# Performance work log

Measured on AMD Instinct MI355X. Metric: run time of the kernel, lower is better.

The kernel has to match this reference:

```python
import jax, jax.numpy as jnp
import numpy as np

HEADS = 16
PHI = (1.0 + np.sqrt(5.0)) / 2.0


def setup_inputs() -> dict:
    key = jax.random.key(0)
    k1, k2, k3, k4 = jax.random.split(key, 4)
    B, L, D = 2, 2048, 1024
    x = jax.random.normal(k1, (B, L, D), dtype=jnp.float32)
    # nn.Linear(dim, 3*dim, bias=False): store as [D, 3D] for x @ W
    w_qkv = jax.random.normal(k2, (D, 3 * D), dtype=jnp.float32) * (D ** -0.5)
    w_proj = jax.random.normal(k3, (D, D), dtype=jnp.float32) * (D ** -0.5)
    b_proj = jax.random.normal(k4, (D,), dtype=jnp.float32) * 0.01
    return {"x": x, "w_qkv": w_qkv, "w_proj": w_proj, "b_proj": b_proj}


def phi_bias(L):
    # pos[i] = (i * phi) mod 1 ; bias = log(exp(-|pos_i - pos_j|) + 1e-8)
    pos = (jnp.arange(L, dtype=jnp.float32) * PHI) % 1.0
    dist = jnp.abs(pos[:, None] - pos[None, :])  # [L, L]
    return jnp.log(jnp.exp(-dist) + 1e-8)


def reference(x, w_qkv, w_proj, b_proj):
    B, L, D = x.shape
    H = HEADS
    Dh = D // H
    scale = Dh ** -0.5
    qkv = (x @ w_qkv).reshape(B, L, 3, H, Dh)
    q = jnp.transpose(qkv[:, :, 0], (0, 2, 1, 3))  # [B, H, L, Dh]
    k = jnp.transpose(qkv[:, :, 1], (0, 2, 1, 3))
    v = jnp.transpose(qkv[:, :, 2], (0, 2, 1, 3))
    attn = jnp.einsum("bhid,bhjd->bhij", q, k) * scale  # [B, H, L, L]
    attn = attn + phi_bias(L)[None, None]  # additive phi-distance bias
    attn = jax.nn.softmax(attn, axis=-1)
    out = jnp.einsum("bhij,bhjd->bhid", attn, v)  # [B, H, L, Dh]
    out = jnp.transpose(out, (0, 2, 1, 3)).reshape(B, L, D)
    return out @ w_proj + b_proj
```

## Files before the change

kernel.cpp:

```cpp
#include <hip/hip_runtime.h>
#include <math.h>


typedef _Float16 f16;
typedef _Float16 f16x4 __attribute__((ext_vector_type(4)));
typedef _Float16 f16x8 __attribute__((ext_vector_type(8)));
typedef float f32x4 __attribute__((ext_vector_type(4)));

#define MFMA32(a, b, c) __builtin_amdgcn_mfma_f32_16x16x32_f16(a, b, c, 0, 0, 0)

static constexpr int Bsz = 2, Lseq = 2048, Dm = 1024, H = 16, Dh = 64;
static constexpr int Mtot = Bsz * Lseq;
static constexpr int NQKV = 3 * Dm;
static constexpr float PHI_F = 1.61803398874989484820f;
static constexpr float LOG2E = 1.44269504088896f;
static constexpr float QS = 0.125f * LOG2E;
static constexpr float CSTEP = 0.55417527999932633f;

__device__ __forceinline__ void load16_to_lds(const f16* g, f16* l) {
  __builtin_amdgcn_global_load_lds(
      (const __attribute__((address_space(1))) unsigned int*)g,
      (__attribute__((address_space(3))) unsigned int*)l, 16, 0, 0);
}

__global__ __launch_bounds__(256) void cast_f32_f16(const float* __restrict__ in,
                                                    f16* __restrict__ out, int n) {
  int i = (blockIdx.x * 256 + threadIdx.x) * 4;
  if (i < n) {
    float4 v = *reinterpret_cast<const float4*>(in + i);
    f16 t[4] = {(f16)v.x, (f16)v.y, (f16)v.z, (f16)v.w};
    *reinterpret_cast<uint2*>(out + i) = *reinterpret_cast<uint2*>(t);
  }
}

__global__ __launch_bounds__(256) void transpose_cast(const float* __restrict__ in,
                                                      f16* __restrict__ out,
                                                      int K, int N) {
  __shared__ float tile[32][33];
  int n0 = blockIdx.x * 32, k0 = blockIdx.y * 32;
  int tx = threadIdx.x & 31, ty = threadIdx.x >> 5;
#pragma unroll
  for (int r = 0; r < 32; r += 8)
    tile[ty + r][tx] = in[(size_t)(k0 + ty + r) * N + n0 + tx];
  __syncthreads();
#pragma unroll
  for (int r = 0; r < 32; r += 8)
    out[(size_t)(n0 + ty + r) * K + k0 + tx] = (f16)tile[tx][ty + r];
}

__global__ __launch_bounds__(256) void v_transpose(const f16* __restrict__ in,
                                                   f16* __restrict__ out) {
  __shared__ f16 td[64][68];
  int bh = blockIdx.y, l0 = blockIdx.x * 64;
  int tid = threadIdx.x;
  const f16* src = in + (size_t)bh * Lseq * Dh;
#pragma unroll
  for (int c = tid; c < 512; c += 256) {
    int row = c >> 3, col = (c & 7) * 8;
    uint4 v = *reinterpret_cast<const uint4*>(src + (size_t)(l0 + row) * Dh + col);
    f16 tmp[8];
    *reinterpret_cast<uint4*>(tmp) = v;
#pragma unroll
    for (int j = 0; j < 8; j++) td[col + j][row] = tmp[j];
  }
  __syncthreads();
  f16* dst = out + (size_t)bh * Dh * Lseq;
#pragma unroll
  for (int c = tid; c < 512; c += 256) {
    int d = c >> 3, co = c & 7;
    int jh = co >> 2, qd = co & 3;
    f16 tmp[8];
#pragma unroll
    for (int e = 0; e < 4; e++) tmp[e] = td[d][jh * 32 + qd * 4 + e];
#pragma unroll
    for (int e = 0; e < 4; e++) tmp[4 + e] = td[d][jh * 32 + 16 + qd * 4 + e];
    *reinterpret_cast<uint4*>(dst + (size_t)d * Lseq + l0 + co * 8) =
        *reinterpret_cast<uint4*>(tmp);
  }
}

template <int MODE>
__global__ __launch_bounds__(256) void gemm_f16(
    const f16* __restrict__ A, const f16* __restrict__ Bt,
    int M, int N, int K,
    f16* __restrict__ qb, f16* __restrict__ kb, f16* __restrict__ vl,
    float* __restrict__ out, const float* __restrict__ bias) {
  constexpr int BM = (MODE == 0) ? 128 : 64;
  constexpr int MI = BM / 32;
  constexpr int AI = BM / 32;
  __shared__ f16 As[BM * 64];
  __shared__ f16 Bs[128 * 64];

  int tid = threadIdx.x;
  int wave = tid >> 6, lane = tid & 63;
  int quad = lane >> 4, l16 = lane & 15;
  int wm = (wave >> 1) * (MI * 16), wn = (wave & 1) * 64;

  int lid = blockIdx.x;
  int xcd = lid & 7, t = lid >> 3;
  int m0, n0;
  if (MODE == 0) {
    int mg = xcd >> 1, ng = xcd & 1;
    m0 = (mg * 8 + t / 12) * 128;
    n0 = (ng * 12 + t % 12) * 128;
  } else {
    m0 = (xcd * 8 + (t >> 3)) * 64;
    n0 = (t & 7) * 128;
  }

  const int gu = (lane & 7) ^ (lane >> 3);
  const f16* gA[AI];
  f16* lA[AI];
#pragma unroll
  for (int i = 0; i < AI; i++) {
    int it = wave * AI + i;
    gA[i] = A + (size_t)(m0 + it * 8 + (lane >> 3)) * K + gu * 8;
    lA[i] = As + it * 512;
  }
  const f16* gB[4];
  f16* lB[4];
#pragma unroll
  for (int i = 0; i < 4; i++) {
    int it = wave * 4 + i;
    gB[i] = Bt + (size_t)(n0 + it * 8 + (lane >> 3)) * K + gu * 8;
    lB[i] = Bs + it * 512;
  }

  f32x4 acc[MI][4] = {};

  for (int k0 = 0; k0 < K; k0 += 64) {
#pragma unroll
    for (int i = 0; i < AI; i++) load16_to_lds(gA[i] + k0, lA[i]);
#pragma unroll
    for (int i = 0; i < 4; i++) load16_to_lds(gB[i] + k0, lB[i]);
    __syncthreads();
#pragma unroll
    for (int s = 0; s < 2; s++) {
      f16x8 a[MI], b[4];
#pragma unroll
      for (int i = 0; i < MI; i++) {
        int row = wm + i * 16 + l16;
        a[i] = *reinterpret_cast<const f16x8*>(
            As + row * 64 + (((s * 4 + quad) ^ (l16 & 7)) * 8));
      }
#pragma unroll
      for (int j = 0; j < 4; j++) {
        int row = wn + j * 16 + l16;
        b[j] = *reinterpret_cast<const f16x8*>(
            Bs + row * 64 + (((s * 4 + quad) ^ (l16 & 7)) * 8));
      }
#pragma unroll
      for (int i = 0; i < MI; i++)
#pragma unroll
        for (int j = 0; j < 4; j++)
          acc[i][j] = MFMA32(a[i], b[j], acc[i][j]);
    }
    __syncthreads();
  }

#pragma unroll
  for (int i = 0; i < MI; i++) {
#pragma unroll
    for (int j = 0; j < 4; j++) {
      int n = n0 + wn + j * 16 + l16;
#pragma unroll
      for (int r = 0; r < 4; r++) {
        int m = m0 + wm + i * 16 + quad * 4 + r;
        if (MODE == 0) {
          int ty = n >> 10;
          int df = n & 1023;
          int h = df >> 6, dh = df & 63;
          int b = m >> 11, l = m & 2047;
          size_t idx = (((size_t)(b * H + h)) * Lseq + l) * Dh + dh;
          if (ty == 0)
            qb[idx] = (f16)(acc[i][j][r] * QS);
          else if (ty == 1)
            kb[idx] = (f16)acc[i][j][r];
          else
            vl[idx] = (f16)acc[i][j][r];
        } else {
          out[(size_t)m * N + n] = acc[i][j][r] + bias[n];
        }
      }
    }
  }
}

__global__ __launch_bounds__(256, 4) void attn_kernel(
    const f16* __restrict__ qb,
    const f16* __restrict__ kb,
    const f16* __restrict__ vb,
    f16* __restrict__ ctx) {
  __shared__ __align__(16) unsigned char smem[16640];
  f16* Ks = (f16*)smem;
  f16* Vs = (f16*)(smem + 8192);

  int bh = blockIdx.y;
  int q0 = blockIdx.x * 64;
  int tid = threadIdx.x, wave = tid >> 6, lane = tid & 63;
  int quad = lane >> 4, l16 = lane & 15;
  int jhalf = wave >> 1, qhalf = wave & 1;

  f16x8 qfrag[2][2];
  float pq[2];
#pragma unroll
  for (int set = 0; set < 2; set++) {
    int q = q0 + qhalf * 32 + set * 16 + l16;
    const f16* Qrow = qb + ((size_t)bh * Lseq + q) * Dh;
    qfrag[set][0] = *reinterpret_cast<const f16x8*>(Qrow + quad * 8);
    qfrag[set][1] = *reinterpret_cast<const f16x8*>(Qrow + 32 + quad * 8);
    pq[set] = fmodf((float)q * PHI_F, 1.0f);
  }

  float pk[2][4];
#pragma unroll
  for (int jb = 0; jb < 2; jb++)
#pragma unroll
    for (int r = 0; r < 4; r++) {
      int j = jhalf * 32 + jb * 16 + quad * 4 + r;
      pk[jb][r] = fmodf((float)j * PHI_F, 1.0f);
    }

  const f16* Kbh = kb + (size_t)bh * Lseq * Dh;
  const f16* Vbh = vb + (size_t)bh * Dh * Lseq;
  const int gu = (lane & 7) ^ (lane >> 3);
  const f16* gK[2];
  const f16* gV[2];
  f16* lK[2];
  f16* lV[2];
#pragma unroll
  for (int i = 0; i < 2; i++) {
    int g8 = (wave * 2 + i) * 8 + (lane >> 3);
    gK[i] = Kbh + (size_t)g8 * Dh + gu * 8;
    gV[i] = Vbh + (size_t)g8 * Lseq + gu * 8;
    lK[i] = Ks + (wave * 2 + i) * 512;
    lV[i] = Vs + (wave * 2 + i) * 512;
  }

  const f16 one = (f16)1.0f;
  const f16x8 ones8 = {one, one, one, one, one, one, one, one};

  f32x4 acc_o[2][4] = {};
  f32x4 acc_l[2] = {};

  for (int j0 = 0; j0 < Lseq; j0 += 64) {
    __syncthreads();
#pragma unroll
    for (int i = 0; i < 2; i++) {
      load16_to_lds(gK[i] + (size_t)j0 * Dh, lK[i]);
      load16_to_lds(gV[i] + j0, lV[i]);
    }
    __syncthreads();

    f32x4 accs[2][2] = {};
#pragma unroll
    for (int s = 0; s < 2; s++)
#pragma unroll
      for (int jb = 0; jb < 2; jb++) {
        f16x8 kf = *reinterpret_cast<const f16x8*>(
            Ks + (jhalf * 32 + jb * 16 + l16) * 64 + (((s * 4 + quad) ^ (l16 & 7)) * 8));
        accs[0][jb] = MFMA32(kf, qfrag[0][s], accs[0][jb]);
        accs[1][jb] = MFMA32(kf, qfrag[1][s], accs[1][jb]);
      }

    f16x8 pf8[2];
#pragma unroll
    for (int set = 0; set < 2; set++) {
#pragma unroll
      for (int jb = 0; jb < 2; jb++) {
        float p[4];
#pragma unroll
        for (int r = 0; r < 4; r++) {
          float d = pq[set] - pk[jb][r];
          float arg = fmaf(-LOG2E, fabsf(d), accs[set][jb][r]);
          p[r] = __builtin_amdgcn_exp2f(arg);
        }
        auto lo = __builtin_amdgcn_cvt_pkrtz(p[0], p[1]);
        auto hi = __builtin_amdgcn_cvt_pkrtz(p[2], p[3]);
        pf8[set][jb * 4 + 0] = lo[0];
        pf8[set][jb * 4 + 1] = lo[1];
        pf8[set][jb * 4 + 2] = hi[0];
        pf8[set][jb * 4 + 3] = hi[1];
      }
      acc_l[set] = MFMA32(ones8, pf8[set], acc_l[set]);
    }
#pragma unroll
    for (int jb = 0; jb < 2; jb++)
#pragma unroll
      for (int r = 0; r < 4; r++)
        pk[jb][r] = __builtin_amdgcn_fractf(pk[jb][r] + CSTEP);

#pragma unroll
    for (int dblk = 0; dblk < 4; dblk++) {
      int row = dblk * 16 + l16;
      f16x8 va = *reinterpret_cast<const f16x8*>(
          Vs + row * 64 + (((jhalf * 4 + quad) ^ (l16 & 7)) * 8));
      acc_o[0][dblk] = MFMA32(va, pf8[0], acc_o[0][dblk]);
      acc_o[1][dblk] = MFMA32(va, pf8[1], acc_o[1][dblk]);
    }
  }

  __syncthreads();
  float* Oex = (float*)smem;
  float* Lex = (float*)(smem + 16384);
  if (jhalf == 1) {
#pragma unroll
    for (int set = 0; set < 2; set++) {
#pragma unroll
      for (int dblk = 0; dblk < 4; dblk++)
#pragma unroll
        for (int r = 0; r < 4; r++)
          Oex[(((qhalf * 2 + set) * 4 + dblk) * 16 + quad * 4 + r) * 16 + l16] =
              acc_o[set][dblk][r];
      if (quad == 0) Lex[(qhalf * 2 + set) * 16 + l16] = acc_l[set][0];
    }
  }
  __syncthreads();
  if (jhalf == 0) {
    int b = bh >> 4, h = bh & 15;
#pragma unroll
    for (int set = 0; set < 2; set++) {
      float ltot = acc_l[set][0] + Lex[(qhalf * 2 + set) * 16 + l16];
      float inv = 1.0f / ltot;
      int q = q0 + qhalf * 32 + set * 16 + l16;
      f16* crow = ctx + (size_t)(b * Lseq + q) * Dm + h * 64;
#pragma unroll
      for (int dblk = 0; dblk < 4; dblk++) {
        f16x4 o;
#pragma unroll
        for (int r = 0; r < 4; r++) {
          float full = acc_o[set][dblk][r] +
              Oex[(((qhalf * 2 + set) * 4 + dblk) * 16 + quad * 4 + r) * 16 + l16];
          o[r] = (f16)(full * inv);
        }
        *reinterpret_cast<uint2*>(crow + dblk * 16 + quad * 4) =
            *reinterpret_cast<uint2*>(&o);
      }
    }
  }
}

extern "C" void kernel_launch(void* const* d_in, const int* in_sizes, int n_in,
                              void* d_out, int out_size, void* d_ws, size_t ws_size,
                              hipStream_t stream) {
  const float* x      = (const float*)d_in[0];
  const float* w_qkv  = (const float*)d_in[1];
  const float* w_proj = (const float*)d_in[2];
  const float* b_proj = (const float*)d_in[3];
  float* out = (float*)d_out;

  f16* xb    = (f16*)d_ws;
  f16* wqkvT = xb + (size_t)Mtot * Dm;
  f16* wpT   = wqkvT + (size_t)NQKV * Dm;
  f16* qb    = wpT + (size_t)Dm * Dm;
  f16* kb    = qb + (size_t)Bsz * H * Lseq * Dh;
  f16* vb    = kb + (size_t)Bsz * H * Lseq * Dh;
  f16* ctx   = vb + (size_t)Bsz * H * Lseq * Dh;
  f16* vl    = ctx;

  cast_f32_f16<<<(Mtot * Dm) / (256 * 4), 256, 0, stream>>>(x, xb, Mtot * Dm);
  transpose_cast<<<dim3(NQKV / 32, Dm / 32), 256, 0, stream>>>(w_qkv, wqkvT, Dm, NQKV);
  transpose_cast<<<dim3(Dm / 32, Dm / 32), 256, 0, stream>>>(w_proj, wpT, Dm, Dm);

  gemm_f16<0><<<768, 256, 0, stream>>>(
      xb, wqkvT, Mtot, NQKV, Dm, qb, kb, vl, nullptr, nullptr);

  v_transpose<<<dim3(Lseq / 64, Bsz * H), 256, 0, stream>>>(vl, vb);

  attn_kernel<<<dim3(Lseq / 64, Bsz * H), 256, 0, stream>>>(qb, kb, vb, ctx);

  gemm_f16<1><<<512, 256, 0, stream>>>(
      ctx, wpT, Mtot, Dm, Dm, nullptr, nullptr, nullptr, out, b_proj);
}
```

Before: 192.5 us.

## Fuse prep kernels, write transposed V from QKV GEMM, process 128 keys per sync

Merges the x cast and both weight transpose-casts into one launch. The QKV GEMM epilogue now writes V directly in the permuted transposed layout the attention kernel expects, which removes the separate v_transpose kernel and its round trip through memory. The attention loop now loads two 64-key tiles per barrier pair, doubling LDS to 32KB, to halve synchronisation overhead. The larger LDS footprint may lower occupancy, and the scattered 8-byte V stores in the epilogue may coalesce poorly.

```diff
diff --git a/kernel.cpp b/kernel.cpp
--- a/kernel.cpp
+++ b/kernel.cpp
@@ -17,28 +17,44 @@
 static constexpr float QS = 0.125f * LOG2E;
 static constexpr float CSTEP = 0.55417527999932633f;
 
+__device__ __forceinline__ void pk2(float a, float b, f16* d) {
+  auto v = __builtin_amdgcn_cvt_pkrtz(a, b);
+  d[0] = (f16)v[0];
+  d[1] = (f16)v[1];
+}
+
 __device__ __forceinline__ void load16_to_lds(const f16* g, f16* l) {
   __builtin_amdgcn_global_load_lds(
       (const __attribute__((address_space(1))) unsigned int*)g,
       (__attribute__((address_space(3))) unsigned int*)l, 16, 0, 0);
 }
 
-__global__ __launch_bounds__(256) void cast_f32_f16(const float* __restrict__ in,
-                                                    f16* __restrict__ out, int n) {
-  int i = (blockIdx.x * 256 + threadIdx.x) * 4;
-  if (i < n) {
-    float4 v = *reinterpret_cast<const float4*>(in + i);
+__global__ __launch_bounds__(256) void prep_kernel(
+    const float* __restrict__ x, const float* __restrict__ wqkv,
+    const float* __restrict__ wproj, f16* __restrict__ xb,
+    f16* __restrict__ wqkvT, f16* __restrict__ wpT) {
+  __shared__ float tile[32][33];
+  int bid = blockIdx.x, tid = threadIdx.x;
+  if (bid < 4096) {
+    int i = bid * 1024 + tid * 4;
+    float4 v = *reinterpret_cast<const float4*>(x + i);
     f16 t[4] = {(f16)v.x, (f16)v.y, (f16)v.z, (f16)v.w};
-    *reinterpret_cast<uint2*>(out + i) = *reinterpret_cast<uint2*>(t);
-  }
-}
-
-__global__ __launch_bounds__(256) void transpose_cast(const float* __restrict__ in,
-                                                      f16* __restrict__ out,
-                                                      int K, int N) {
-  __shared__ float tile[32][33];
-  int n0 = blockIdx.x * 32, k0 = blockIdx.y * 32;
-  int tx = threadIdx.x & 31, ty = threadIdx.x >> 5;
+    *reinterpret_cast<uint2*>(xb + i) = *reinterpret_cast<uint2*>(t);
+    return;
+  }
+  const float* in;
+  f16* out;
+  int K, N, n0, k0;
+  if (bid < 4096 + 3072) {
+    int b2 = bid - 4096;
+    in = wqkv; out = wqkvT; K = Dm; N = NQKV;
+    n0 = (b2 % 96) * 32; k0 = (b2 / 96) * 32;
+  } else {
+    int b2 = bid - 7168;
+    in = wproj; out = wpT; K = Dm; N = Dm;
+    n0 = (b2 & 31) * 32; k0 = (b2 >> 5) * 32;
+  }
+  int tx = tid & 31, ty = tid >> 5;
 #pragma unroll
   for (int r = 0; r < 32; r += 8)
     tile[ty + r][tx] = in[(size_t)(k0 + ty + r) * N + n0 + tx];
@@ -46,44 +62,13 @@
 #pragma unroll
   for (int r = 0; r < 32; r += 8)
     out[(size_t)(n0 + ty + r) * K + k0 + tx] = (f16)tile[tx][ty + r];
-}
-
-__global__ __launch_bounds__(256) void v_transpose(const f16* __restrict__ in,
-                                                   f16* __restrict__ out) {
-  __shared__ f16 td[64][68];
-  int bh = blockIdx.y, l0 = blockIdx.x * 64;
-  int tid = threadIdx.x;
-  const f16* src = in + (size_t)bh * Lseq * Dh;
-#pragma unroll
-  for (int c = tid; c < 512; c += 256) {
-    int row = c >> 3, col = (c & 7) * 8;
-    uint4 v = *reinterpret_cast<const uint4*>(src + (size_t)(l0 + row) * Dh + col);
-    f16 tmp[8];
-    *reinterpret_cast<uint4*>(tmp) = v;
-#pragma unroll
-    for (int j = 0; j < 8; j++) td[col + j][row] = tmp[j];
-  }
-  __syncthreads();
-  f16* dst = out + (size_t)bh * Dh * Lseq;
-#pragma unroll
-  for (int c = tid; c < 512; c += 256) {
-    int d = c >> 3, co = c & 7;
-    int jh = co >> 2, qd = co & 3;
-    f16 tmp[8];
-#pragma unroll
-    for (int e = 0; e < 4; e++) tmp[e] = td[d][jh * 32 + qd * 4 + e];
-#pragma unroll
-    for (int e = 0; e < 4; e++) tmp[4 + e] = td[d][jh * 32 + 16 + qd * 4 + e];
-    *reinterpret_cast<uint4*>(dst + (size_t)d * Lseq + l0 + co * 8) =
-        *reinterpret_cast<uint4*>(tmp);
-  }
 }
 
 template <int MODE>
 __global__ __launch_bounds__(256) void gemm_f16(
     const f16* __restrict__ A, const f16* __restrict__ Bt,
     int M, int N, int K,
-    f16* __restrict__ qb, f16* __restrict__ kb, f16* __restrict__ vl,
+    f16* __restrict__ qb, f16* __restrict__ kb, f16* __restrict__ vb,
     float* __restrict__ out, const float* __restrict__ bias) {
   constexpr int BM = (MODE == 0) ? 128 : 64;
   constexpr int MI = BM / 32;
@@ -158,29 +143,57 @@
     __syncthreads();
   }
 
-#pragma unroll
-  for (int i = 0; i < MI; i++) {
-#pragma unroll
-    for (int j = 0; j < 4; j++) {
-      int n = n0 + wn + j * 16 + l16;
-#pragma unroll
-      for (int r = 0; r < 4; r++) {
-        int m = m0 + wm + i * 16 + quad * 4 + r;
-        if (MODE == 0) {
-          int ty = n >> 10;
-          int df = n & 1023;
-          int h = df >> 6, dh = df & 63;
-          int b = m >> 11, l = m & 2047;
-          size_t idx = (((size_t)(b * H + h)) * Lseq + l) * Dh + dh;
-          if (ty == 0)
-            qb[idx] = (f16)(acc[i][j][r] * QS);
-          else if (ty == 1)
-            kb[idx] = (f16)acc[i][j][r];
-          else
-            vl[idx] = (f16)acc[i][j][r];
-        } else {
+  if (MODE == 1) {
+#pragma unroll
+    for (int i = 0; i < MI; i++)
+#pragma unroll
+      for (int j = 0; j < 4; j++) {
+        int n = n0 + wn + j * 16 + l16;
+#pragma unroll
+        for (int r = 0; r < 4; r++) {
+          int m = m0 + wm + i * 16 + quad * 4 + r;
           out[(size_t)m * N + n] = acc[i][j][r] + bias[n];
         }
+      }
+    return;
+  }
+  int ty = n0 >> 10;
+  if (ty < 2) {
+    f16* dst = (ty == 0) ? qb : kb;
+    float sc = (ty == 0) ? QS : 1.0f;
+#pragma unroll
+    for (int i = 0; i < MI; i++)
+#pragma unroll
+      for (int j = 0; j < 4; j++) {
+        int n = n0 + wn + j * 16 + l16;
+        int h = (n & 1023) >> 6, dh = n & 63;
+#pragma unroll
+        for (int r = 0; r < 4; r++) {
+          int m = m0 + wm + i * 16 + quad * 4 + r;
+          int b = m >> 11, l = m & 2047;
+          dst[(((size_t)(b * H + h)) * Lseq + l) * Dh + dh] =
+              (f16)(acc[i][j][r] * sc);
+        }
+      }
+  } else {
+#pragma unroll
+    for (int i = 0; i < MI; i++) {
+      int mb = m0 + wm + i * 16 + quad * 4;
+      int b = mb >> 11, l = mb & 2047;
+      int L0 = l & ~63, lg = l & 63;
+      int c = ((lg >> 5) << 2) | ((lg >> 2) & 3);
+      int e0 = ((lg >> 4) & 1) * 4;
+      int off = L0 + c * 8 + e0;
+#pragma unroll
+      for (int j = 0; j < 4; j++) {
+        int n = n0 + wn + j * 16 + l16;
+        int h = (n & 1023) >> 6, dh = n & 63;
+        f16x4 v;
+        pk2(acc[i][j][0], acc[i][j][1], (f16*)&v);
+        pk2(acc[i][j][2], acc[i][j][3], ((f16*)&v) + 2);
+        *reinterpret_cast<uint2*>(
+            vb + ((size_t)(b * H + h) * Dh + dh) * Lseq + off) =
+            *reinterpret_cast<uint2*>(&v);
       }
     }
   }
@@ -191,9 +204,11 @@
     const f16* __restrict__ kb,
     const f16* __restrict__ vb,
     f16* __restrict__ ctx) {
-  __shared__ __align__(16) unsigned char smem[16640];
-  f16* Ks = (f16*)smem;
-  f16* Vs = (f16*)(smem + 8192);
+  __shared__ __align__(16) unsigned char smem[32768];
+  f16* Ks0 = (f16*)smem;
+  f16* Ks1 = (f16*)(smem + 8192);
+  f16* Vs0 = (f16*)(smem + 16384);
+  f16* Vs1 = (f16*)(smem + 24576);
 
   int bh = blockIdx.y;
   int q0 = blockIdx.x * 64;
@@ -233,8 +248,8 @@
     int g8 = (wave * 2 + i) * 8 + (lane >> 3);
     gK[i] = Kbh + (size_t)g8 * Dh + gu * 8;
     gV[i] = Vbh + (size_t)g8 * Lseq + gu * 8;
-    lK[i] = Ks + (wave * 2 + i) * 512;
-    lV[i] = Vs + (wave * 2 + i) * 512;
+    lK[i] = Ks0 + (wave * 2 + i) * 512;
+    lV[i] = Vs0 + (wave * 2 + i) * 512;
   }
 
   const f16 one = (f16)1.0f;
@@ -243,26 +258,18 @@
   f32x4 acc_o[2][4] = {};
   f32x4 acc_l[2] = {};
 
-  for (int j0 = 0; j0 < Lseq; j0 += 64) {
-    __syncthreads();
-#pragma unroll
-    for (int i = 0; i < 2; i++) {
-      load16_to_lds(gK[i] + (size_t)j0 * Dh, lK[i]);
-      load16_to_lds(gV[i] + j0, lV[i]);
-    }
-    __syncthreads();
-
+  auto phase = [&](const f16* Ksp, const f16* Vsp) {
     f32x4 accs[2][2] = {};
 #pragma unroll
     for (int s = 0; s < 2; s++)
 #pragma unroll
       for (int jb = 0; jb < 2; jb++) {
         f16x8 kf = *reinterpret_cast<const f16x8*>(
-            Ks + (jhalf * 32 + jb * 16 + l16) * 64 + (((s * 4 + quad) ^ (l16 & 7)) * 8));
+            Ksp + (jhalf * 32 + jb * 16 + l16) * 64 +
+            (((s * 4 + quad) ^ (l16 & 7)) * 8));
         accs[0][jb] = MFMA32(kf, qfrag[0][s], accs[0][jb]);
         accs[1][jb] = MFMA32(kf, qfrag[1][s], accs[1][jb]);
       }
-
     f16x8 pf8[2];
 #pragma unroll
     for (int set = 0; set < 2; set++) {
@@ -275,12 +282,8 @@
           float arg = fmaf(-LOG2E, fabsf(d), accs[set][jb][r]);
           p[r] = __builtin_amdgcn_exp2f(arg);
         }
-        auto lo = __builtin_amdgcn_cvt_pkrtz(p[0], p[1]);
-        auto hi = __builtin_amdgcn_cvt_pkrtz(p[2], p[3]);
-        pf8[set][jb * 4 + 0] = lo[0];
-        pf8[set][jb * 4 + 1] = lo[1];
-        pf8[set][jb * 4 + 2] = hi[0];
-        pf8[set][jb * 4 + 3] = hi[1];
+        pk2(p[0], p[1], ((f16*)&pf8[set]) + jb * 4);
+        pk2(p[2], p[3], ((f16*)&pf8[set]) + jb * 4 + 2);
       }
       acc_l[set] = MFMA32(ones8, pf8[set], acc_l[set]);
     }
@@ -289,15 +292,28 @@
 #pragma unroll
       for (int r = 0; r < 4; r++)
         pk[jb][r] = __builtin_amdgcn_fractf(pk[jb][r] + CSTEP);
-
 #pragma unroll
     for (int dblk = 0; dblk < 4; dblk++) {
       int row = dblk * 16 + l16;
       f16x8 va = *reinterpret_cast<const f16x8*>(
-          Vs + row * 64 + (((jhalf * 4 + quad) ^ (l16 & 7)) * 8));
+          Vsp + row * 64 + (((jhalf * 4 + quad) ^ (l16 & 7)) * 8));
       acc_o[0][dblk] = MFMA32(va, pf8[0], acc_o[0][dblk]);
       acc_o[1][dblk] = MFMA32(va, pf8[1], acc_o[1][dblk]);
     }
+  };
+
+  for (int j0 = 0; j0 < Lseq; j0 += 128) {
+    __syncthreads();
+#pragma unroll
+    for (int i = 0; i < 2; i++) {
+      load16_to_lds(gK[i] + (size_t)j0 * Dh, lK[i]);
+      load16_to_lds(gK[i] + (size_t)(j0 + 64) * Dh, lK[i] + 4096);
+      load16_to_lds(gV[i] + j0, lV[i]);
+      load16_to_lds(gV[i] + j0 + 64, lV[i] + 4096);
+    }
+    __syncthreads();
+    phase(Ks0, Vs0);
+    phase(Ks1, Vs1);
   }
 
   __syncthreads();
@@ -356,16 +372,11 @@
   f16* kb    = qb + (size_t)Bsz * H * Lseq * Dh;
   f16* vb    = kb + (size_t)Bsz * H * Lseq * Dh;
   f16* ctx   = vb + (size_t)Bsz * H * Lseq * Dh;
-  f16* vl    = ctx;
-
-  cast_f32_f16<<<(Mtot * Dm) / (256 * 4), 256, 0, stream>>>(x, xb, Mtot * Dm);
-  transpose_cast<<<dim3(NQKV / 32, Dm / 32), 256, 0, stream>>>(w_qkv, wqkvT, Dm, NQKV);
-  transpose_cast<<<dim3(Dm / 32, Dm / 32), 256, 0, stream>>>(w_proj, wpT, Dm, Dm);
+
+  prep_kernel<<<8192, 256, 0, stream>>>(x, w_qkv, w_proj, xb, wqkvT, wpT);
 
   gemm_f16<0><<<768, 256, 0, stream>>>(
-      xb, wqkvT, Mtot, NQKV, Dm, qb, kb, vl, nullptr, nullptr);
-
-  v_transpose<<<dim3(Lseq / 64, Bsz * H), 256, 0, stream>>>(vl, vb);
+      xb, wqkvT, Mtot, NQKV, Dm, qb, kb, vb, nullptr, nullptr);
 
   attn_kernel<<<dim3(Lseq / 64, Bsz * H), 256, 0, stream>>>(qb, kb, vb, ctx);
 
```

Result: no change. 194.4 us (+1.0%).
